# Kernel tuning notes

Measured on AMD Instinct MI355X. Metric: run time of the kernel, lower is better.

Reference implementation:

```python
import jax, jax.numpy as jnp
import numpy as np

B, TV, TS, DIN, D = 32, 1024, 64, 1024, 512
EPS = 1e-15


def setup_inputs() -> dict:
    key = jax.random.key(0)
    k1, k2, k3, k4, k5, k6 = jax.random.split(key, 6)
    videos = jax.random.normal(k1, (B, TV, DIN), dtype=jnp.float32)
    sentences = jax.random.normal(k2, (B, TS, DIN), dtype=jnp.float32)
    lengths = jax.random.randint(k3, (B,), 1, TS, dtype=jnp.int32)
    scale = 1.0 / np.sqrt(DIN)
    Wv = jax.random.normal(k4, (DIN, D), dtype=jnp.float32) * scale
    bv = jnp.zeros((D,), dtype=jnp.float32)
    Ws = jax.random.normal(k5, (DIN, D), dtype=jnp.float32) * scale
    bs = jnp.zeros((D,), dtype=jnp.float32)
    return {"videos": videos, "sentences": sentences, "lengths": lengths,
            "Wv": Wv, "bv": bv, "Ws": Ws, "bs": bs}


def _pair_score(V, S):
    # V: [TV, D] video repr for item i; S: [TS, D] sentence repr for item j
    nv = jnp.linalg.norm(V, axis=1)                      # [TV]
    ns = jnp.linalg.norm(S, axis=1)                      # [TS]
    # cosine-similarity coattention matrix via normalized matmul (no repeat/tile)
    C = (V @ S.T) / (nv[:, None] * ns[None, :] + EPS)    # [TV, TS]
    A = jax.nn.softmax(C, axis=1)                        # normalize over sentence axis
    att = A @ S                                          # [TV, D] sentence attention
    num = jnp.sum(V * att, axis=1)                       # [TV]
    den = nv * jnp.linalg.norm(att, axis=1)
    score = num / (den + EPS)                            # [TV] per-frame video score
    return jax.nn.logsumexp(score)                       # scalar


def reference(videos, sentences, lengths, Wv, bv, Ws, bs):
    # per-timestep dense encoders (video_layer / sentence_layer)
    videos_repr = jnp.einsum('btf,fd->btd', videos, Wv) + bv      # [B, TV, D]
    sentences_repr = jnp.einsum('bsf,fd->bsd', sentences, Ws) + bs  # [B, TS, D]
    # all-pairs (i video, j sentence) scores, vectorized over the B x B grid
    pairwise = jax.vmap(lambda V: jax.vmap(lambda S: _pair_score(V, S))(sentences_repr))
    scores_videos = pairwise(videos_repr)                # [B, B]
    return scores_videos
```

## Files before the change

kernel.cpp:

```cpp
#include <hip/hip_runtime.h>
#include <hip/hip_bf16.h>
#include <stdint.h>
#include <math.h>

typedef __attribute__((ext_vector_type(8))) __bf16 bf16x8;
typedef __attribute__((ext_vector_type(4))) float f32x4;

#define B_   32
#define TV_  1024
#define TS_  64
#define DIN_ 1024
#define D_   512

static __device__ __forceinline__ unsigned short f2bf(float f) {
    union { float f; uint32_t u; } x; x.f = f;
    uint32_t r = x.u + 0x7fffu + ((x.u >> 16) & 1u);
    return (unsigned short)(r >> 16);
}
static __device__ __forceinline__ uint32_t cvtpk(float lo, float hi) {
    uint32_t r;
    asm("v_cvt_pk_bf16_f32 %0, %1, %2" : "=v"(r) : "v"(lo), "v"(hi));
    return r;
}
static __device__ __forceinline__ void swap32(uint32_t& a, uint32_t& b) {
    asm volatile("v_permlane32_swap_b32 %0, %1" : "+v"(a), "+v"(b));
}
static __device__ __forceinline__ void swap16(uint32_t& a, uint32_t& b) {
    asm volatile("v_permlane16_swap_b32 %0, %1" : "+v"(a), "+v"(b));
}

__global__ __launch_bounds__(256) void transpose_w(const float* __restrict__ Wv,
                                                   const float* __restrict__ Wsn,
                                                   unsigned short* __restrict__ Wt) {
    const int w = blockIdx.z;
    const float* src = w ? Wsn : Wv;
    __shared__ float t[32][33];
    const int k0 = blockIdx.x * 32, n0 = blockIdx.y * 32;
    const int tx = threadIdx.x & 31, ty = threadIdx.x >> 5;
    #pragma unroll
    for (int r = 0; r < 32; r += 8)
        t[r + ty][tx] = src[(size_t)(k0 + r + ty) * D_ + n0 + tx];
    __syncthreads();
    #pragma unroll
    for (int r = 0; r < 32; r += 8)
        Wt[(size_t)w * 524288 + (size_t)(n0 + r + ty) * DIN_ + k0 + tx] = f2bf(t[tx][r + ty]);
}

__global__ __launch_bounds__(256) void encoder_gemm(const float* __restrict__ X,
                                                    const unsigned short* __restrict__ Wt,
                                                    const float* __restrict__ bias,
                                                    unsigned short* __restrict__ outR,
                                                    int mpx) {
    __shared__ char Asb[128 * 128];
    __shared__ char Bsb[128 * 128];
    const int bid = blockIdx.x;
    const int xcd = bid & 7, sl = bid >> 3;
    const int m0 = (xcd * mpx + (sl >> 2)) * 128;
    const int n0 = (sl & 3) * 128;
    const int tid = threadIdx.x;
    const int lane = tid & 63, wid = tid >> 6;
    const int g = lane >> 4, c = lane & 15;
    const int wm = wid >> 1, wn = wid & 1;

    f32x4 acc[4][4];
    {
        f32x4 z = {0.f, 0.f, 0.f, 0.f};
        #pragma unroll
        for (int a = 0; a < 4; ++a)
            #pragma unroll
            for (int b = 0; b < 4; ++b) acc[a][b] = z;
    }

    for (int kk = 0; kk < 16; ++kk) {
        const int k0 = kk * 64;
        #pragma unroll
        for (int it = 0; it < 8; ++it) {
            int idx = it * 256 + tid;
            int m = idx >> 4, k4 = idx & 15;
            float4 v = *(const float4*)(X + (size_t)(m0 + m) * DIN_ + k0 + k4 * 4);
            uint2 pk;
            pk.x = ((uint32_t)f2bf(v.y) << 16) | f2bf(v.x);
            pk.y = ((uint32_t)f2bf(v.w) << 16) | f2bf(v.z);
            *(uint2*)(Asb + m * 128 + ((k4 * 8) ^ ((m & 7) << 4))) = pk;
        }
        #pragma unroll
        for (int it = 0; it < 4; ++it) {
            int idx = it * 256 + tid;
            int n = idx >> 3, kq = idx & 7;
            uint4 v = *(const uint4*)(Wt + (size_t)(n0 + n) * DIN_ + k0 + kq * 8);
            *(uint4*)(Bsb + n * 128 + ((kq * 16) ^ ((n & 7) << 4))) = v;
        }
        __syncthreads();
        #pragma unroll
        for (int ks = 0; ks < 2; ++ks) {
            bf16x8 a[4], b[4];
            #pragma unroll
            for (int mt = 0; mt < 4; ++mt) {
                int row = wm * 64 + mt * 16 + c;
                a[mt] = *(const bf16x8*)(Asb + row * 128 + ((g * 16 + ks * 64) ^ ((c & 7) << 4)));
            }
            #pragma unroll
            for (int nt = 0; nt < 4; ++nt) {
                int rowb = wn * 64 + nt * 16 + c;
                b[nt] = *(const bf16x8*)(Bsb + rowb * 128 + ((g * 16 + ks * 64) ^ ((c & 7) << 4)));
            }
            #pragma unroll
            for (int mt = 0; mt < 4; ++mt)
                #pragma unroll
                for (int nt = 0; nt < 4; ++nt)
                    acc[mt][nt] = __builtin_amdgcn_mfma_f32_16x16x32_bf16(a[mt], b[nt], acc[mt][nt], 0, 0, 0);
        }
        __syncthreads();
    }
    #pragma unroll
    for (int nt = 0; nt < 4; ++nt) {
        int col = n0 + wn * 64 + nt * 16 + c;
        float bb = bias[col];
        #pragma unroll
        for (int mt = 0; mt < 4; ++mt) {
            int rbase = m0 + wm * 64 + mt * 16 + g * 4;
            #pragma unroll
            for (int r = 0; r < 4; ++r)
                outR[(size_t)(rbase + r) * D_ + col] = f2bf(acc[mt][nt][r] + bb);
        }
    }
}

__global__ __launch_bounds__(256) void rownorm_kernel(const unsigned short* __restrict__ R,
                                                      float* __restrict__ nrm, int nrows) {
    const int row = blockIdx.x * 4 + (threadIdx.x >> 6);
    const int lane = threadIdx.x & 63;
    if (row >= nrows) return;
    uint4 v = ((const uint4*)(R + (size_t)row * D_))[lane];
    float s = 0.f;
    uint32_t wsx[4] = {v.x, v.y, v.z, v.w};
    #pragma unroll
    for (int q = 0; q < 4; ++q) {
        float lo = __uint_as_float(wsx[q] << 16);
        float hi = __uint_as_float(wsx[q] & 0xffff0000u);
        s += lo * lo + hi * hi;
    }
    #pragma unroll
    for (int d = 1; d < 64; d <<= 1) s += __shfl_xor(s, d);
    if (lane == 0) nrm[row] = sqrtf(s);
}

__global__ __launch_bounds__(256) void gram_kernel(const unsigned short* __restrict__ S,
                                                   unsigned short* __restrict__ Gn,
                                                   unsigned short* __restrict__ Sf,
                                                   float* __restrict__ lgns) {
    const int i = blockIdx.x;
    const int tid = threadIdx.x, lane = tid & 63, w = tid >> 6;
    const int g = lane >> 4, c = lane & 15;
    const unsigned short* Sp = S + (size_t)i * TS_ * D_;
    __shared__ float rns_sh[64];

    {
        const int row = tid >> 2, q = tid & 3;
        const uint4* rp = (const uint4*)(Sp + (size_t)row * D_ + q * 128);
        float s = 0.f;
        #pragma unroll
        for (int e = 0; e < 16; ++e) {
            uint4 v = rp[e];
            uint32_t wsx[4] = {v.x, v.y, v.z, v.w};
            #pragma unroll
            for (int qq = 0; qq < 4; ++qq) {
                float lo = __uint_as_float(wsx[qq] << 16);
                float hi = __uint_as_float(wsx[qq] & 0xffff0000u);
                s += lo * lo + hi * hi;
            }
        }
        s += __shfl_xor(s, 1);
        s += __shfl_xor(s, 2);
        if (q == 0) {
            rns_sh[row] = rsqrtf(s);
            lgns[i * 64 + row] = 0.5f * log2f(s);
        }
    }
    __syncthreads();

    {
        f32x4 acc[4];
        {
            f32x4 z = {0.f, 0.f, 0.f, 0.f};
            #pragma unroll
            for (int a = 0; a < 4; ++a) acc[a] = z;
        }
        #pragma unroll
        for (int ks = 0; ks < 16; ++ks) {
            bf16x8 a = *(const bf16x8*)(Sp + (size_t)(w * 16 + c) * D_ + ks * 32 + g * 8);
            #pragma unroll
            for (int nt = 0; nt < 4; ++nt) {
                bf16x8 b = *(const bf16x8*)(Sp + (size_t)(nt * 16 + c) * D_ + ks * 32 + g * 8);
                acc[nt] = __builtin_amdgcn_mfma_f32_16x16x32_bf16(a, b, acc[nt], 0, 0, 0);
            }
        }
        #pragma unroll
        for (int nt = 0; nt < 4; ++nt)
            #pragma unroll
            for (int r = 0; r < 4; ++r) {
                int R = w * 16 + g * 4 + r, C = nt * 16 + c;
                float vn = acc[nt][r] * rns_sh[R] * rns_sh[C];
                int idx = (w * 2 + (nt >> 1)) * 512 + (((nt & 1) * 2 + (c >> 3)) * 16 + g * 4 + r) * 8 + (c & 7);
                Gn[(size_t)i * 4096 + idx] = f2bf(vn);
            }
    }

    #pragma unroll
    for (int t = 0; t < 16; ++t) {
        int idx = t * 256 + tid;
        int ks = idx >> 8, at = (idx >> 6) & 3, ln = idx & 63;
        int row = at * 16 + (ln & 15), gg = ln >> 4;
        uint4 raw = *(const uint4*)(Sp + (size_t)row * D_ + ks * 32 + gg * 8);
        float sc = rns_sh[row];
        uint32_t rw[4] = {raw.x, raw.y, raw.z, raw.w};
        uint4 o;
        uint32_t* op = (uint32_t*)&o;
        #pragma unroll
        for (int q = 0; q < 4; ++q) {
            float lo = __uint_as_float(rw[q] << 16) * sc;
            float hi = __uint_as_float(rw[q] & 0xffff0000u) * sc;
            op[q] = cvtpk(lo, hi);
        }
        *(uint4*)(Sf + (size_t)i * 32768 + idx * 8) = o;
    }
}

__global__ __launch_bounds__(512) void pairwise_kernel(const unsigned short* __restrict__ V,
                                                       const unsigned short* __restrict__ Sf,
                                                       const unsigned short* __restrict__ Gn,
                                                       const float* __restrict__ nv,
                                                       const float* __restrict__ lgns,
                                                       float* __restrict__ outp) {
    __shared__ char Ssh[131072];
    __shared__ char Gsh[16384];
    __shared__ float lgsh[128];
    __shared__ float wsum[16];

    const int bid = blockIdx.x;
    const int xcd = bid & 7, slot = bid >> 3;
    const int i = xcd + 8 * (slot >> 4);
    const int jp = slot & 15;
    const int tid = threadIdx.x;
    const int lane = tid & 63, w = tid >> 6;
    const int g = lane >> 4, c = lane & 15;
    const float L2E = 1.4426950408889634f;

    {
        const unsigned short* Sjf = Sf + (size_t)jp * 65536;
        #pragma unroll
        for (int it = 0; it < 16; ++it) {
            int idx = it * 512 + tid;
            *(uint4*)(Ssh + idx * 16) = *(const uint4*)(Sjf + idx * 8);
        }
        const unsigned short* Gp = Gn + (size_t)jp * 8192;
        #pragma unroll
        for (int it = 0; it < 2; ++it) {
            int idx = it * 512 + tid;
            *(uint4*)(Gsh + idx * 16) = *(const uint4*)(Gp + idx * 8);
        }
        if (tid < 32) *(float4*)(lgsh + tid * 4) = *(const float4*)(lgns + jp * 128 + tid * 4);
    }
    __syncthreads();

    const unsigned short* Vb[4];
    #pragma unroll
    for (int mt = 0; mt < 4; ++mt)
        Vb[mt] = V + ((size_t)i * TV_ + w * 64 + mt * 16 + c) * D_ + g * 8;
    const float* nvb = nv + i * TV_ + w * 64 + c;

    float s_run0 = 0.0f, s_run1 = 0.0f;

    for (int chunk = 0; chunk < 2; ++chunk) {
        const size_t coff = (size_t)chunk * 512 * D_;
        f32x4 acc[4][8];
        {
            f32x4 z = {0.f, 0.f, 0.f, 0.f};
            #pragma unroll
            for (int a = 0; a < 4; ++a)
                #pragma unroll
                for (int b = 0; b < 8; ++b) acc[a][b] = z;
        }
        bf16x8 bcur[4], bnxt[4];
        #pragma unroll
        for (int mt = 0; mt < 4; ++mt) bcur[mt] = *(const bf16x8*)(Vb[mt] + coff);
        #pragma unroll
        for (int ks = 0; ks < 16; ++ks) {
            bf16x8 a[8];
            #pragma unroll
            for (int q = 0; q < 8; ++q)
                a[q] = *(const bf16x8*)(Ssh + ((q >> 2) << 16) + (((ks * 4 + (q & 3))) << 10) + lane * 16);
            if (ks < 15) {
                #pragma unroll
                for (int mt = 0; mt < 4; ++mt)
                    bnxt[mt] = *(const bf16x8*)(Vb[mt] + coff + (ks + 1) * 32);
            }
            __builtin_amdgcn_s_setprio(1);
            #pragma unroll
            for (int mt = 0; mt < 4; ++mt)
                #pragma unroll
                for (int q = 0; q < 8; ++q)
                    acc[mt][q] = __builtin_amdgcn_mfma_f32_16x16x32_bf16(a[q], bcur[mt], acc[mt][q], 0, 0, 0);
            __builtin_amdgcn_s_setprio(0);
            #pragma unroll
            for (int mt = 0; mt < 4; ++mt) bcur[mt] = bnxt[mt];
        }

        float nv4[4], rnv[4];
        #pragma unroll
        for (int mt = 0; mt < 4; ++mt) {
            nv4[mt] = nvb[chunk * 512 + mt * 16];
            rnv[mt] = __builtin_amdgcn_rcpf(nv4[mt]);
        }

        #pragma unroll
        for (int jj = 0; jj < 2; ++jj) {
            float lg[16];
            #pragma unroll
            for (int at = 0; at < 4; ++at) {
                float4 t4 = *(const float4*)(lgsh + jj * 64 + at * 16 + g * 4);
                lg[at * 4 + 0] = t4.x; lg[at * 4 + 1] = t4.y;
                lg[at * 4 + 2] = t4.z; lg[at * 4 + 3] = t4.w;
            }
            float SPC[4], SPQ[4] = {0.f, 0.f, 0.f, 0.f};

            #pragma unroll
            for (int half = 0; half < 2; ++half) {
                uint32_t bfr[2][2][4];
                #pragma unroll
                for (int m2 = 0; m2 < 2; ++m2) {
                    const int mt = half * 2 + m2;
                    float rnvL = rnv[mt] * L2E;
                    float SPCm = 0.f;
                    #pragma unroll
                    for (int at = 0; at < 4; ++at)
                        #pragma unroll
                        for (int r = 0; r < 4; ++r) {
                            float t = acc[mt][jj * 4 + at][r];
                            float e = exp2f(fmaf(t, rnvL, lg[at * 4 + r]));
                            SPCm = fmaf(e, t, SPCm);
                            acc[mt][jj * 4 + at][r] = e;
                        }
                    SPC[mt] = SPCm;
                    #pragma unroll
                    for (int ks2 = 0; ks2 < 2; ++ks2) {
                        const int a0 = jj * 4 + ks2 * 2, a1 = a0 + 1;
                        uint32_t A  = cvtpk(acc[mt][a0][0], acc[mt][a0][1]);
                        uint32_t Bw = cvtpk(acc[mt][a0][2], acc[mt][a0][3]);
                        uint32_t C  = cvtpk(acc[mt][a1][0], acc[mt][a1][1]);
                        uint32_t Dw = cvtpk(acc[mt][a1][2], acc[mt][a1][3]);
                        swap32(A, C);  swap16(A, C);
                        swap32(Bw, Dw); swap16(Bw, Dw);
                        bfr[m2][ks2][0] = A;  bfr[m2][ks2][1] = Bw;
                        bfr[m2][ks2][2] = C;  bfr[m2][ks2][3] = Dw;
                    }
                }
                #pragma unroll
                for (int st = 0; st < 4; ++st) {
                    bf16x8 g0 = *(const bf16x8*)(Gsh + (jj << 13) + ((st * 2 + 0) << 10) + lane * 16);
                    bf16x8 g1 = *(const bf16x8*)(Gsh + (jj << 13) + ((st * 2 + 1) << 10) + lane * 16);
                    __builtin_amdgcn_s_setprio(1);
                    #pragma unroll
                    for (int m2 = 0; m2 < 2; ++m2) {
                        const int mt = half * 2 + m2;
                        union { uint32_t u[4]; bf16x8 v; } f0, f1;
                        #pragma unroll
                        for (int q = 0; q < 4; ++q) { f0.u[q] = bfr[m2][0][q]; f1.u[q] = bfr[m2][1][q]; }
                        f32x4 d2 = {0.f, 0.f, 0.f, 0.f};
                        d2 = __builtin_amdgcn_mfma_f32_16x16x32_bf16(g0, f0.v, d2, 0, 0, 0);
                        d2 = __builtin_amdgcn_mfma_f32_16x16x32_bf16(g1, f1.v, d2, 0, 0, 0);
                        #pragma unroll
                        for (int r = 0; r < 4; ++r) SPQ[mt] += acc[mt][jj * 4 + st][r] * d2[r];
                    }
                    __builtin_amdgcn_s_setprio(0);
                }
            }

            #pragma unroll
            for (int mt = 0; mt < 4; ++mt) {
                float SPCm = SPC[mt], SPQm = SPQ[mt];
                SPCm += __shfl_xor(SPCm, 16); SPCm += __shfl_xor(SPCm, 32);
                SPQm += __shfl_xor(SPQm, 16); SPQm += __shfl_xor(SPQm, 32);
                float sc = SPCm * rnv[mt] * rsqrtf(fmaxf(SPQm, 1e-20f));
                float ev = exp2f(sc * L2E);
                if (jj == 0) s_run0 += ev; else s_run1 += ev;
            }
        }
    }

    #pragma unroll
    for (int d = 1; d < 16; d <<= 1) {
        s_run0 += __shfl_xor(s_run0, d);
        s_run1 += __shfl_xor(s_run1, d);
    }
    if (lane == 0) { wsum[w * 2] = s_run0; wsum[w * 2 + 1] = s_run1; }
    __syncthreads();
    if (tid < 2) {
        float total = 0.f;
        #pragma unroll
        for (int ww = 0; ww < 8; ++ww) total += wsum[ww * 2 + tid];
        outp[i * 32 + jp * 2 + tid] = 0.69314718055994531f * log2f(total);
    }
}

extern "C" void kernel_launch(void* const* d_in, const int* in_sizes, int n_in,
                              void* d_out, int out_size, void* d_ws, size_t ws_size,
                              hipStream_t stream) {
    const float* videos    = (const float*)d_in[0];
    const float* sentences = (const float*)d_in[1];
    const float* Wv  = (const float*)d_in[3];
    const float* bv  = (const float*)d_in[4];
    const float* Wsn = (const float*)d_in[5];
    const float* bs  = (const float*)d_in[6];
    float* outp = (float*)d_out;

    char* ws = (char*)d_ws;
    unsigned short* Vrep = (unsigned short*)(ws);
    unsigned short* Srep = (unsigned short*)(ws + 33554432);
    unsigned short* Wt   = (unsigned short*)(ws + 35651584);
    unsigned short* Gn   = (unsigned short*)(ws + 37748736);
    float*          nv   = (float*)(ws + 38010880);
    float*          lgns = (float*)(ws + 38141952);
    unsigned short* Sf   = Wt;

    transpose_w<<<dim3(32, 16, 2), 256, 0, stream>>>(Wv, Wsn, Wt);
    encoder_gemm<<<1024, 256, 0, stream>>>(videos, Wt, bv, Vrep, 32);
    encoder_gemm<<<64, 256, 0, stream>>>(sentences, Wt + 524288, bs, Srep, 2);
    rownorm_kernel<<<8192, 256, 0, stream>>>(Vrep, nv, B_ * TV_);
    gram_kernel<<<B_, 256, 0, stream>>>(Srep, Gn, Sf, lgns);
    pairwise_kernel<<<512, 512, 0, stream>>>(Vrep, Sf, Gn, nv, lgns, outp);
}
```

Baseline: 208.6 us.

## Merge encoder launches, use direct-to-LDS weight loads, shrink pairwise per-wave tile

Combines the video and sentence encoder GEMMs into one launch that picks its operands by block index. The weight tile now loads straight into LDS via global_load_lds, which drops the XOR swizzle, and the fp32-to-bf16 packing uses v_cvt_pk_bf16_f32. The pairwise kernel halves rows per wave (2 m-tiles, 4 chunks) and declares launch_bounds(512,2) to cut register pressure. Risks: unswizzled B reads may cause LDS bank conflicts, and the large LDS footprint may still limit occupancy to one block per CU.

New measurement: 189.2 us. 1.1x faster.

```diff
diff --git a/kernel.cpp b/kernel.cpp
--- a/kernel.cpp
+++ b/kernel.cpp
@@ -27,6 +27,10 @@
 }
 static __device__ __forceinline__ void swap16(uint32_t& a, uint32_t& b) {
     asm volatile("v_permlane16_swap_b32 %0, %1" : "+v"(a), "+v"(b));
+}
+static __device__ __forceinline__ void gload16(const void* g, void* l) {
+    __builtin_amdgcn_global_load_lds((const __attribute__((address_space(1))) uint32_t*)g,
+                                     (__attribute__((address_space(3))) uint32_t*)l, 16, 0, 0);
 }
 
 __global__ __launch_bounds__(256) void transpose_w(const float* __restrict__ Wv,
@@ -46,17 +50,29 @@
         Wt[(size_t)w * 524288 + (size_t)(n0 + r + ty) * DIN_ + k0 + tx] = f2bf(t[tx][r + ty]);
 }
 
-__global__ __launch_bounds__(256) void encoder_gemm(const float* __restrict__ X,
+__global__ __launch_bounds__(256) void encoder_gemm(const float* __restrict__ videos,
+                                                    const float* __restrict__ sentences,
                                                     const unsigned short* __restrict__ Wt,
-                                                    const float* __restrict__ bias,
-                                                    unsigned short* __restrict__ outR,
-                                                    int mpx) {
+                                                    const float* __restrict__ bv,
+                                                    const float* __restrict__ bs,
+                                                    unsigned short* __restrict__ Vrep,
+                                                    unsigned short* __restrict__ Srep) {
     __shared__ char Asb[128 * 128];
     __shared__ char Bsb[128 * 128];
     const int bid = blockIdx.x;
-    const int xcd = bid & 7, sl = bid >> 3;
-    const int m0 = (xcd * mpx + (sl >> 2)) * 128;
-    const int n0 = (sl & 3) * 128;
+    const float* X; const unsigned short* W; const float* bias; unsigned short* out;
+    int m0, n0;
+    if (bid < 1024) {
+        int xcd = bid & 7, sl = bid >> 3;
+        m0 = (xcd * 32 + (sl >> 2)) * 128;
+        n0 = (sl & 3) * 128;
+        X = videos; W = Wt; bias = bv; out = Vrep;
+    } else {
+        int sb = bid - 1024;
+        m0 = (sb >> 2) * 128;
+        n0 = (sb & 3) * 128;
+        X = sentences; W = Wt + 524288; bias = bs; out = Srep;
+    }
     const int tid = threadIdx.x;
     const int lane = tid & 63, wid = tid >> 6;
     const int g = lane >> 4, c = lane & 15;
@@ -79,16 +95,15 @@
             int m = idx >> 4, k4 = idx & 15;
             float4 v = *(const float4*)(X + (size_t)(m0 + m) * DIN_ + k0 + k4 * 4);
             uint2 pk;
-            pk.x = ((uint32_t)f2bf(v.y) << 16) | f2bf(v.x);
-            pk.y = ((uint32_t)f2bf(v.w) << 16) | f2bf(v.z);
+            pk.x = cvtpk(v.x, v.y);
+            pk.y = cvtpk(v.z, v.w);
             *(uint2*)(Asb + m * 128 + ((k4 * 8) ^ ((m & 7) << 4))) = pk;
         }
         #pragma unroll
-        for (int it = 0; it < 4; ++it) {
-            int idx = it * 256 + tid;
-            int n = idx >> 3, kq = idx & 7;
-            uint4 v = *(const uint4*)(Wt + (size_t)(n0 + n) * DIN_ + k0 + kq * 8);
-            *(uint4*)(Bsb + n * 128 + ((kq * 16) ^ ((n & 7) << 4))) = v;
+        for (int t = 0; t < 4; ++t) {
+            int row = wid * 32 + t * 8 + (lane >> 3);
+            const unsigned short* src = W + (size_t)(n0 + row) * DIN_ + k0 + (lane & 7) * 8;
+            gload16(src, Bsb + wid * 4096 + t * 1024);
         }
         __syncthreads();
         #pragma unroll
@@ -102,7 +117,7 @@
             #pragma unroll
             for (int nt = 0; nt < 4; ++nt) {
                 int rowb = wn * 64 + nt * 16 + c;
-                b[nt] = *(const bf16x8*)(Bsb + rowb * 128 + ((g * 16 + ks * 64) ^ ((c & 7) << 4)));
+                b[nt] = *(const bf16x8*)(Bsb + rowb * 128 + (g * 16 + ks * 64));
             }
             #pragma unroll
             for (int mt = 0; mt < 4; ++mt)
@@ -121,7 +136,7 @@
             int rbase = m0 + wm * 64 + mt * 16 + g * 4;
             #pragma unroll
             for (int r = 0; r < 4; ++r)
-                outR[(size_t)(rbase + r) * D_ + col] = f2bf(acc[mt][nt][r] + bb);
+                out[(size_t)(rbase + r) * D_ + col] = f2bf(acc[mt][nt][r] + bb);
         }
     }
 }
@@ -226,12 +241,12 @@
     }
 }
 
-__global__ __launch_bounds__(512) void pairwise_kernel(const unsigned short* __restrict__ V,
-                                                       const unsigned short* __restrict__ Sf,
-                                                       const unsigned short* __restrict__ Gn,
-                                                       const float* __restrict__ nv,
-                                                       const float* __restrict__ lgns,
-                                                       float* __restrict__ outp) {
+__global__ __launch_bounds__(512, 2) void pairwise_kernel(const unsigned short* __restrict__ V,
+                                                          const unsigned short* __restrict__ Sf,
+                                                          const unsigned short* __restrict__ Gn,
+                                                          const float* __restrict__ nv,
+                                                          const float* __restrict__ lgns,
+                                                          float* __restrict__ outp) {
     __shared__ char Ssh[131072];
     __shared__ char Gsh[16384];
     __shared__ float lgsh[128];
@@ -263,27 +278,27 @@
     }
     __syncthreads();
 
-    const unsigned short* Vb[4];
-    #pragma unroll
-    for (int mt = 0; mt < 4; ++mt)
-        Vb[mt] = V + ((size_t)i * TV_ + w * 64 + mt * 16 + c) * D_ + g * 8;
-    const float* nvb = nv + i * TV_ + w * 64 + c;
+    const unsigned short* Vb[2];
+    #pragma unroll
+    for (int mt = 0; mt < 2; ++mt)
+        Vb[mt] = V + ((size_t)i * TV_ + w * 32 + mt * 16 + c) * D_ + g * 8;
+    const float* nvb = nv + i * TV_ + w * 32 + c;
 
     float s_run0 = 0.0f, s_run1 = 0.0f;
 
-    for (int chunk = 0; chunk < 2; ++chunk) {
-        const size_t coff = (size_t)chunk * 512 * D_;
-        f32x4 acc[4][8];
+    for (int chunk = 0; chunk < 4; ++chunk) {
+        const size_t coff = (size_t)chunk * 256 * D_;
+        f32x4 acc[2][8];
         {
             f32x4 z = {0.f, 0.f, 0.f, 0.f};
             #pragma unroll
-            for (int a = 0; a < 4; ++a)
+            for (int a = 0; a < 2; ++a)
                 #pragma unroll
                 for (int b = 0; b < 8; ++b) acc[a][b] = z;
         }
-        bf16x8 bcur[4], bnxt[4];
-        #pragma unroll
-        for (int mt = 0; mt < 4; ++mt) bcur[mt] = *(const bf16x8*)(Vb[mt] + coff);
+        bf16x8 bcur[2], bnxt[2];
+        #pragma unroll
+        for (int mt = 0; mt < 2; ++mt) bcur[mt] = *(const bf16x8*)(Vb[mt] + coff);
         #pragma unroll
         for (int ks = 0; ks < 16; ++ks) {
             bf16x8 a[8];
@@ -292,24 +307,24 @@
                 a[q] = *(const bf16x8*)(Ssh + ((q >> 2) << 16) + (((ks * 4 + (q & 3))) << 10) + lane * 16);
             if (ks < 15) {
                 #pragma unroll
-                for (int mt = 0; mt < 4; ++mt)
+                for (int mt = 0; mt < 2; ++mt)
                     bnxt[mt] = *(const bf16x8*)(Vb[mt] + coff + (ks + 1) * 32);
             }
             __builtin_amdgcn_s_setprio(1);
             #pragma unroll
-            for (int mt = 0; mt < 4; ++mt)
+            for (int mt = 0; mt < 2; ++mt)
                 #pragma unroll
                 for (int q = 0; q < 8; ++q)
                     acc[mt][q] = __builtin_amdgcn_mfma_f32_16x16x32_bf16(a[q], bcur[mt], acc[mt][q], 0, 0, 0);
             __builtin_amdgcn_s_setprio(0);
             #pragma unroll
-            for (int mt = 0; mt < 4; ++mt) bcur[mt] = bnxt[mt];
-        }
-
-        float nv4[4], rnv[4];
-        #pragma unroll
-        for (int mt = 0; mt < 4; ++mt) {
-            nv4[mt] = nvb[chunk * 512 + mt * 16];
+            for (int mt = 0; mt < 2; ++mt) bcur[mt] = bnxt[mt];
+        }
+
+        float nv4[2], rnv[2];
+        #pragma unroll
+        for (int mt = 0; mt < 2; ++mt) {
+            nv4[mt] = nvb[chunk * 256 + mt * 16];
             rnv[mt] = __builtin_amdgcn_rcpf(nv4[mt]);
         }
 
@@ -322,62 +337,56 @@
                 lg[at * 4 + 0] = t4.x; lg[at * 4 + 1] = t4.y;
                 lg[at * 4 + 2] = t4.z; lg[at * 4 + 3] = t4.w;
             }
-            float SPC[4], SPQ[4] = {0.f, 0.f, 0.f, 0.f};
-
-            #pragma unroll
-            for (int half = 0; half < 2; ++half) {
-                uint32_t bfr[2][2][4];
-                #pragma unroll
-                for (int m2 = 0; m2 < 2; ++m2) {
-                    const int mt = half * 2 + m2;
-                    float rnvL = rnv[mt] * L2E;
-                    float SPCm = 0.f;
+            float SPC[2], SPQ[2] = {0.f, 0.f};
+            uint32_t bfr[2][2][4];
+            #pragma unroll
+            for (int mt = 0; mt < 2; ++mt) {
+                float rnvL = rnv[mt] * L2E;
+                float SPCm = 0.f;
+                #pragma unroll
+                for (int at = 0; at < 4; ++at)
                     #pragma unroll
-                    for (int at = 0; at < 4; ++at)
-                        #pragma unroll
-                        for (int r = 0; r < 4; ++r) {
-                            float t = acc[mt][jj * 4 + at][r];
-                            float e = exp2f(fmaf(t, rnvL, lg[at * 4 + r]));
-                            SPCm = fmaf(e, t, SPCm);
-                            acc[mt][jj * 4 + at][r] = e;
-                        }
-                    SPC[mt] = SPCm;
+                    for (int r = 0; r < 4; ++r) {
+                        float t = acc[mt][jj * 4 + at][r];
+                        float e = exp2f(fmaf(t, rnvL, lg[at * 4 + r]));
+                        SPCm = fmaf(e, t, SPCm);
+                        acc[mt][jj * 4 + at][r] = e;
+                    }
+                SPC[mt] = SPCm;
+                #pragma unroll
+                for (int ks2 = 0; ks2 < 2; ++ks2) {
+                    const int a0 = jj * 4 + ks2 * 2, a1 = a0 + 1;
+                    uint32_t A  = cvtpk(acc[mt][a0][0], acc[mt][a0][1]);
+                    uint32_t Bw = cvtpk(acc[mt][a0][2], acc[mt][a0][3]);
+                    uint32_t C  = cvtpk(acc[mt][a1][0], acc[mt][a1][1]);
+                    uint32_t Dw = cvtpk(acc[mt][a1][2], acc[mt][a1][3]);
+                    swap32(A, C);  swap16(A, C);
+                    swap32(Bw, Dw); swap16(Bw, Dw);
+                    bfr[mt][ks2][0] = A;  bfr[mt][ks2][1] = Bw;
+                    bfr[mt][ks2][2] = C;  bfr[mt][ks2][3] = Dw;
+                }
+            }
+            #pragma unroll
+            for (int st = 0; st < 4; ++st) {
+                bf16x8 g0 = *(const bf16x8*)(Gsh + (jj << 13) + ((st * 2 + 0) << 10) + lane * 16);
+                bf16x8 g1 = *(const bf16x8*)(Gsh + (jj << 13) + ((st * 2 + 1) << 10) + lane * 16);
+                __builtin_amdgcn_s_setprio(1);
+                #pragma unroll
+                for (int mt = 0; mt < 2; ++mt) {
+                    union { uint32_t u[4]; bf16x8 v; } f0, f1;
                     #pragma unroll
-                    for (int ks2 = 0; ks2 < 2; ++ks2) {
-                        const int a0 = jj * 4 + ks2 * 2, a1 = a0 + 1;
-                        uint32_t A  = cvtpk(acc[mt][a0][0], acc[mt][a0][1]);
-                        uint32_t Bw = cvtpk(acc[mt][a0][2], acc[mt][a0][3]);
-                        uint32_t C  = cvtpk(acc[mt][a1][0], acc[mt][a1][1]);
-                        uint32_t Dw = cvtpk(acc[mt][a1][2], acc[mt][a1][3]);
-                        swap32(A, C);  swap16(A, C);
-                        swap32(Bw, Dw); swap16(Bw, Dw);
-                        bfr[m2][ks2][0] = A;  bfr[m2][ks2][1] = Bw;
-                        bfr[m2][ks2][2] = C;  bfr[m2][ks2][3] = Dw;
-                    }
+                    for (int q = 0; q < 4; ++q) { f0.u[q] = bfr[mt][0][q]; f1.u[q] = bfr[mt][1][q]; }
+                    f32x4 d2 = {0.f, 0.f, 0.f, 0.f};
+                    d2 = __builtin_amdgcn_mfma_f32_16x16x32_bf16(g0, f0.v, d2, 0, 0, 0);
+                    d2 = __builtin_amdgcn_mfma_f32_16x16x32_bf16(g1, f1.v, d2, 0, 0, 0);
+                    #pragma unroll
+                    for (int r = 0; r < 4; ++r) SPQ[mt] += acc[mt][jj * 4 + st][r] * d2[r];
                 }
-                #pragma unroll
-                for (int st = 0; st < 4; ++st) {
-                    bf16x8 g0 = *(const bf16x8*)(Gsh + (jj << 13) + ((st * 2 + 0) << 10) + lane * 16);
-                    bf16x8 g1 = *(const bf16x8*)(Gsh + (jj << 13) + ((st * 2 + 1) << 10) + lane * 16);
-                    __builtin_amdgcn_s_setprio(1);
-                    #pragma unroll
-                    for (int m2 = 0; m2 < 2; ++m2) {
-                        const int mt = half * 2 + m2;
-                        union { uint32_t u[4]; bf16x8 v; } f0, f1;
-                        #pragma unroll
-                        for (int q = 0; q < 4; ++q) { f0.u[q] = bfr[m2][0][q]; f1.u[q] = bfr[m2][1][q]; }
-                        f32x4 d2 = {0.f, 0.f, 0.f, 0.f};
-                        d2 = __builtin_amdgcn_mfma_f32_16x16x32_bf16(g0, f0.v, d2, 0, 0, 0);
-                        d2 = __builtin_amdgcn_mfma_f32_16x16x32_bf16(g1, f1.v, d2, 0, 0, 0);
-                        #pragma unroll
-                        for (int r = 0; r < 4; ++r) SPQ[mt] += acc[mt][jj * 4 + st][r] * d2[r];
-                    }
-                    __builtin_amdgcn_s_setprio(0);
-                }
-            }
-
-            #pragma unroll
-            for (int mt = 0; mt < 4; ++mt) {
+                __builtin_amdgcn_s_setprio(0);
+            }
+
+            #pragma unroll
+            for (int mt = 0; mt < 2; ++mt) {
                 float SPCm = SPC[mt], SPQm = SPQ[mt];
                 SPCm += __shfl_xor(SPCm, 16); SPCm += __shfl_xor(SPCm, 32);
                 SPQm += __shfl_xor(SPQm, 16); SPQm += __shfl_xor(SPQm, 32);
@@ -424,8 +433,7 @@
     unsigned short* Sf   = Wt;
 
     transpose_w<<<dim3(32, 16, 2), 256, 0, stream>>>(Wv, Wsn, Wt);
-    encoder_gemm<<<1024, 256, 0, stream>>>(videos, Wt, bv, Vrep, 32);
-    encoder_gemm<<<64, 256, 0, stream>>>(sentences, Wt + 524288, bs, Srep, 2);
+    encoder_gemm<<<1088, 256, 0, stream>>>(videos, sentences, Wt, bv, bs, Vrep, Srep);
     rownorm_kernel<<<8192, 256, 0, stream>>>(Vrep, nv, B_ * TV_);
     gram_kernel<<<B_, 256, 0, stream>>>(Srep, Gn, Sf, lgns);
     pairwise_kernel<<<512, 512, 0, stream>>>(Vrep, Sf, Gn, nv, lgns, outp);
```
